# Performance work log

Hardware: AMD Instinct MI355X
Metric: run time of the kernel (lower is better)

Reference implementation:

```python
import jax, jax.numpy as jnp
import numpy as np

N_NODES = 50000
N_EDGES = 800000
NODE_DIM = 128
EDGE_LBL_DIM = 64
EDGE_FT_OUT_DIM = 128


def setup_inputs() -> dict:
    key = jax.random.key(0)
    k1, k2, k3, k4, k5 = jax.random.split(key, 5)
    h = jax.random.normal(k1, (N_NODES, NODE_DIM), dtype=jnp.float32)
    edge_labels = jax.random.normal(k2, (N_EDGES, EDGE_LBL_DIM), dtype=jnp.float32)
    src = jax.random.randint(k3, (N_EDGES,), 0, N_NODES)
    # learned params: fc (no bias) and e_attn_fc (no bias)
    W_fc = jax.random.normal(k4, (EDGE_LBL_DIM, EDGE_FT_OUT_DIM), dtype=jnp.float32) * 0.05
    W_attn = jax.random.normal(k5, (NODE_DIM + EDGE_FT_OUT_DIM, 1), dtype=jnp.float32) * 0.05
    return {"h": h, "edge_labels": edge_labels, "W_fc": W_fc, "W_attn": W_attn, "src": src}


def reference(h, edge_labels, W_fc, W_attn, src):
    """Edge weighting with segmented softmax grouped by src node.

    e_weighted = fc(edge_labels)                       # [E, F]
    a = e_attn_fc(concat([e_weighted, h[src]]))        # [E, 1]
    e = leaky_relu(a)
    gamma = softmax(e) segmented over edges sharing the same src
    out = gamma * e_weighted                           # [E, F]
    """
    n_nodes = h.shape[0]
    e_w = edge_labels @ W_fc                      # [E, F]
    src_ft = h[src]                               # [E, D] gather
    z2 = jnp.concatenate([e_w, src_ft], axis=-1)  # [E, D+F]
    a = z2 @ W_attn                               # [E, 1]
    e = jax.nn.leaky_relu(a, negative_slope=0.01)
    # segmented (per-src-group) numerically-stable softmax
    m = jax.ops.segment_max(e, src, num_segments=n_nodes)   # [N, 1]
    ex = jnp.exp(e - m[src])
    den = jax.ops.segment_sum(ex, src, num_segments=n_nodes)  # [N, 1]
    gamma = ex / den[src]
    return gamma * e_w
```

## Files before the change

### kernel.cpp

```cpp
#include <hip/hip_runtime.h>

#define N_DIM 128
#define L_DIM 64
#define F_DIM 128

__device__ __forceinline__ float rlane(float x, int l) {
    return __int_as_float(__builtin_amdgcn_readlane(__float_as_int(x), l));
}

__global__ void k_prep(const float* __restrict__ Wfc,
                       const float* __restrict__ Wattn,
                       float* __restrict__ v) {
    int k = threadIdx.x;
    float acc = 0.f;
#pragma unroll 8
    for (int f = 0; f < F_DIM; ++f) acc += Wfc[k * F_DIM + f] * Wattn[f];
    v[k] = acc;
}

__global__ void k_u(const float* __restrict__ h,
                    const float* __restrict__ Wattn,
                    float* __restrict__ u, int N) {
    int lane = threadIdx.x & 63;
    int wid = (int)((blockIdx.x * (unsigned)blockDim.x + threadIdx.x) >> 6);
    int nw  = (int)((gridDim.x * (unsigned)blockDim.x) >> 6);
    float2 wa = *(const float2*)(Wattn + F_DIM + 2 * lane);
    for (int n = wid; n < N; n += nw) {
        float2 hv = *(const float2*)(h + (long)n * N_DIM + 2 * lane);
        float p = hv.x * wa.x + hv.y * wa.y;
#pragma unroll
        for (int off = 32; off > 0; off >>= 1) p += __shfl_xor(p, off, 64);
        if (lane == 0) u[n] = p;
    }
}

__global__ void __launch_bounds__(256) k_se(const float* __restrict__ el,
                                            const float* __restrict__ v,
                                            const float* __restrict__ u,
                                            const int* __restrict__ src,
                                            float* __restrict__ ex_out,
                                            float* __restrict__ den,
                                            int E) {
    const int lane = threadIdx.x & 63;
    const int j16  = lane & 15;
    const int grp  = lane >> 4;
    int wid = (int)((blockIdx.x * (unsigned)blockDim.x + threadIdx.x) >> 6);
    int nw  = (int)((gridDim.x * (unsigned)blockDim.x) >> 6);

    float4 v4 = *(const float4*)(v + 4 * j16);
    const int C = (E + 63) >> 6;

    for (int c = wid; c < C; c += nw) {
        const long e0 = (long)c * 64;
        const int my_e = (int)e0 + 4 * j16 + grp;
        const bool full = (e0 + 64 <= E);

        if (full) {
            int   sv = src[my_e];
            float uu = u[sv];
            float kept = 0.f;
            const float4* elv = (const float4*)(el + e0 * L_DIM);
#pragma unroll
            for (int j = 0; j < 16; ++j) {
                float4 q = elv[j * 64 + lane];
                float p = q.x * v4.x + q.y * v4.y + q.z * v4.z + q.w * v4.w;
                p += __shfl_xor(p, 1, 64);
                p += __shfl_xor(p, 2, 64);
                p += __shfl_xor(p, 4, 64);
                p += __shfl_xor(p, 8, 64);
                float ue = __shfl(uu, (grp << 4) | j, 64);
                float s  = p + ue;
                float ev = fmaxf(s, 0.01f * s);
                float exv = __expf(ev);
                kept = (j16 == j) ? exv : kept;
            }
            ex_out[my_e] = kept;
            atomicAdd(den + sv, kept);
        } else {
            for (int j = 0; j < 16; ++j) {
                long e = e0 + 4 * j + grp;
                if (e >= E) continue;
                const float4* row = (const float4*)(el + e * L_DIM);
                float4 q = row[j16];
                float p = q.x * v4.x + q.y * v4.y + q.z * v4.z + q.w * v4.w;
                p += __shfl_xor(p, 1, 64);
                p += __shfl_xor(p, 2, 64);
                p += __shfl_xor(p, 4, 64);
                p += __shfl_xor(p, 8, 64);
                if (j16 == 0) {
                    int sv2 = src[e];
                    float s = p + u[sv2];
                    float ev = fmaxf(s, 0.01f * s);
                    float exv = __expf(ev);
                    ex_out[e] = exv;
                    atomicAdd(den + sv2, exv);
                }
            }
        }
    }
}

__global__ void __launch_bounds__(256, 1) k_out(const float* __restrict__ el,
                                                const float* __restrict__ Wfc,
                                                const int* __restrict__ src,
                                                const float* __restrict__ ex,
                                                const float* __restrict__ den,
                                                float* __restrict__ out,
                                                int E) {
    const int lane = threadIdx.x & 63;
    const int gw = (int)(blockIdx.x * 4u + (threadIdx.x >> 6));
    const int nw = (int)(gridDim.x * 4u);
    const int G = E >> 2;

    float w0[L_DIM], w1[L_DIM];
#pragma unroll
    for (int k = 0; k < L_DIM; ++k) {
        float2 wv = *(const float2*)(Wfc + k * F_DIM + 2 * lane);
        w0[k] = wv.x;
        w1[k] = wv.y;
    }

    int g = gw;
    if (g >= G) return;

    int gu = __builtin_amdgcn_readfirstlane(g);
    float4 q  = *(const float4*)(el + (long)gu * (4 * L_DIM) + lane * 4);
    float4 x4 = *(const float4*)(ex + 4 * (long)gu);
    int4   s4 = *(const int4*)(src + 4 * (long)gu);

    while (true) {
        const int gn = g + nw;
        const bool more = gn < G;
        float4 qn, x4n; int4 s4n;
        if (more) {
            int gun = __builtin_amdgcn_readfirstlane(gn);
            qn  = *(const float4*)(el + (long)gun * (4 * L_DIM) + lane * 4);
            x4n = *(const float4*)(ex + 4 * (long)gun);
            s4n = *(const int4*)(src + 4 * (long)gun);
        }
        float d0 = den[s4.x], d1 = den[s4.y], d2 = den[s4.z], d3 = den[s4.w];

        float a00 = 0.f, a01 = 0.f, a10 = 0.f, a11 = 0.f;
        float a20 = 0.f, a21 = 0.f, a30 = 0.f, a31 = 0.f;
        const float qa[4] = {q.x, q.y, q.z, q.w};
#pragma unroll
        for (int k = 0; k < L_DIM; ++k) {
            const int ln = k >> 2;
            const float c = qa[k & 3];
            float b0 = rlane(c, ln);
            float b1 = rlane(c, 16 + ln);
            float b2 = rlane(c, 32 + ln);
            float b3 = rlane(c, 48 + ln);
            a00 += b0 * w0[k]; a01 += b0 * w1[k];
            a10 += b1 * w0[k]; a11 += b1 * w1[k];
            a20 += b2 * w0[k]; a21 += b2 * w1[k];
            a30 += b3 * w0[k]; a31 += b3 * w1[k];
        }

        const float g0 = x4.x / d0, g1 = x4.y / d1;
        const float g2 = x4.z / d2, g3 = x4.w / d3;
        const long eb = (long)g * 4;
        *(float2*)(out + (eb + 0) * F_DIM + 2 * lane) = make_float2(g0 * a00, g0 * a01);
        *(float2*)(out + (eb + 1) * F_DIM + 2 * lane) = make_float2(g1 * a10, g1 * a11);
        *(float2*)(out + (eb + 2) * F_DIM + 2 * lane) = make_float2(g2 * a20, g2 * a21);
        *(float2*)(out + (eb + 3) * F_DIM + 2 * lane) = make_float2(g3 * a30, g3 * a31);

        if (!more) break;
        g = gn; q = qn; x4 = x4n; s4 = s4n;
    }
}

extern "C" void kernel_launch(void* const* d_in, const int* in_sizes, int n_in,
                              void* d_out, int out_size, void* d_ws, size_t ws_size,
                              hipStream_t stream) {
    const float* h     = (const float*)d_in[0];
    const float* el    = (const float*)d_in[1];
    const float* Wfc   = (const float*)d_in[2];
    const float* Wattn = (const float*)d_in[3];
    const int*   src   = (const int*)d_in[4];
    float* out = (float*)d_out;

    int N = in_sizes[0] / N_DIM;
    int E = in_sizes[4];

    float* v_ws = (float*)d_ws;
    float* u_ws = (float*)d_ws + 64;
    float* den  = (float*)d_ws + 64 + N;
    float* exb  = (float*)d_ws + 64 + 2 * (size_t)N;

    hipMemsetAsync(den, 0, (size_t)N * sizeof(float), stream);

    k_prep<<<1, 64, 0, stream>>>(Wfc, Wattn, v_ws);
    k_u<<<1024, 256, 0, stream>>>(h, Wattn, u_ws, N);
    k_se<<<1024, 256, 0, stream>>>(el, v_ws, u_ws, src, exb, den, E);
    k_out<<<2048, 256, 0, stream>>>(el, Wfc, src, exb, den, out, E);
}
```

Measured before the change: 744.3 us.

## Replicate softmax denominators per XCC and stage edge rows through LDS

Softmax denominator accumulation now goes to one replica per XCC, using workgroup-scope relaxed atomics, and a new merge kernel sums the replicas. This is meant to cut cross-die atomic contention. The output GEMV now broadcasts edge-label rows through double-buffered LDS instead of 256 readlane operations per group, and the launch-bounds occupancy hint is dropped. The weight-vector precompute is folded into the u kernel, which removes a launch. The risks are the extra merge pass and larger memset, and the assumption that workgroup-scope atomics stay coherent within an XCC.

Measured after the change: 917.6 us. 23.3% more time.

```diff
diff --git a/kernel.cpp b/kernel.cpp
--- a/kernel.cpp
+++ b/kernel.cpp
@@ -3,24 +3,26 @@
 #define N_DIM 128
 #define L_DIM 64
 #define F_DIM 128
-
-__device__ __forceinline__ float rlane(float x, int l) {
-    return __int_as_float(__builtin_amdgcn_readlane(__float_as_int(x), l));
-}
-
-__global__ void k_prep(const float* __restrict__ Wfc,
-                       const float* __restrict__ Wattn,
-                       float* __restrict__ v) {
-    int k = threadIdx.x;
-    float acc = 0.f;
+#define NREP 8
+
+__device__ __forceinline__ int xcc_id() {
+    int x;
+    asm volatile("s_getreg_b32 %0, hwreg(HW_REG_XCC_ID)" : "=s"(x));
+    return x & (NREP - 1);
+}
+
+__global__ void k_u(const float* __restrict__ h,
+                    const float* __restrict__ Wfc,
+                    const float* __restrict__ Wattn,
+                    float* __restrict__ u,
+                    float* __restrict__ v, int N) {
+    if (blockIdx.x == 0 && threadIdx.x < 64) {
+        int k = threadIdx.x;
+        float acc = 0.f;
 #pragma unroll 8
-    for (int f = 0; f < F_DIM; ++f) acc += Wfc[k * F_DIM + f] * Wattn[f];
-    v[k] = acc;
-}
-
-__global__ void k_u(const float* __restrict__ h,
-                    const float* __restrict__ Wattn,
-                    float* __restrict__ u, int N) {
+        for (int f = 0; f < F_DIM; ++f) acc += Wfc[k * F_DIM + f] * Wattn[f];
+        v[k] = acc;
+    }
     int lane = threadIdx.x & 63;
     int wid = (int)((blockIdx.x * (unsigned)blockDim.x + threadIdx.x) >> 6);
     int nw  = (int)((gridDim.x * (unsigned)blockDim.x) >> 6);
@@ -39,13 +41,15 @@
                                             const float* __restrict__ u,
                                             const int* __restrict__ src,
                                             float* __restrict__ ex_out,
-                                            float* __restrict__ den,
-                                            int E) {
+                                            float* __restrict__ den_rep,
+                                            int E, int N) {
     const int lane = threadIdx.x & 63;
     const int j16  = lane & 15;
     const int grp  = lane >> 4;
     int wid = (int)((blockIdx.x * (unsigned)blockDim.x + threadIdx.x) >> 6);
     int nw  = (int)((gridDim.x * (unsigned)blockDim.x) >> 6);
+
+    float* myrep = den_rep + (size_t)xcc_id() * N;
 
     float4 v4 = *(const float4*)(v + 4 * j16);
     const int C = (E + 63) >> 6;
@@ -75,7 +79,8 @@
                 kept = (j16 == j) ? exv : kept;
             }
             ex_out[my_e] = kept;
-            atomicAdd(den + sv, kept);
+            __hip_atomic_fetch_add(myrep + sv, kept, __ATOMIC_RELAXED,
+                                   __HIP_MEMORY_SCOPE_WORKGROUP);
         } else {
             for (int j = 0; j < 16; ++j) {
                 long e = e0 + 4 * j + grp;
@@ -93,22 +98,35 @@
                     float ev = fmaxf(s, 0.01f * s);
                     float exv = __expf(ev);
                     ex_out[e] = exv;
-                    atomicAdd(den + sv2, exv);
+                    __hip_atomic_fetch_add(myrep + sv2, exv, __ATOMIC_RELAXED,
+                                           __HIP_MEMORY_SCOPE_WORKGROUP);
                 }
             }
         }
     }
 }
 
-__global__ void __launch_bounds__(256, 1) k_out(const float* __restrict__ el,
-                                                const float* __restrict__ Wfc,
-                                                const int* __restrict__ src,
-                                                const float* __restrict__ ex,
-                                                const float* __restrict__ den,
-                                                float* __restrict__ out,
-                                                int E) {
+__global__ void k_merge(const float* __restrict__ rep,
+                        float* __restrict__ den, int N) {
+    int i = (int)(blockIdx.x * (unsigned)blockDim.x + threadIdx.x);
+    if (i >= N) return;
+    float s = 0.f;
+#pragma unroll
+    for (int r = 0; r < NREP; ++r) s += rep[(size_t)r * N + i];
+    den[i] = s;
+}
+
+__global__ void __launch_bounds__(256) k_out(const float* __restrict__ el,
+                                             const float* __restrict__ Wfc,
+                                             const int* __restrict__ src,
+                                             const float* __restrict__ ex,
+                                             const float* __restrict__ den,
+                                             float* __restrict__ out,
+                                             int E) {
+    __shared__ float4 sle[2][4][4][16];
     const int lane = threadIdx.x & 63;
-    const int gw = (int)(blockIdx.x * 4u + (threadIdx.x >> 6));
+    const int w    = threadIdx.x >> 6;
+    const int gw = (int)(blockIdx.x * 4u + w);
     const int nw = (int)(gridDim.x * 4u);
     const int G = E >> 2;
 
@@ -123,40 +141,42 @@
     int g = gw;
     if (g >= G) return;
 
-    int gu = __builtin_amdgcn_readfirstlane(g);
-    float4 q  = *(const float4*)(el + (long)gu * (4 * L_DIM) + lane * 4);
-    float4 x4 = *(const float4*)(ex + 4 * (long)gu);
-    int4   s4 = *(const int4*)(src + 4 * (long)gu);
+    float4 q = *(const float4*)(el + (long)g * (4 * L_DIM) + lane * 4);
+    int buf = 0;
+    sle[buf][w][lane >> 4][lane & 15] = q;
 
     while (true) {
         const int gn = g + nw;
         const bool more = gn < G;
-        float4 qn, x4n; int4 s4n;
+        float4 qn;
         if (more) {
-            int gun = __builtin_amdgcn_readfirstlane(gn);
-            qn  = *(const float4*)(el + (long)gun * (4 * L_DIM) + lane * 4);
-            x4n = *(const float4*)(ex + 4 * (long)gun);
-            s4n = *(const int4*)(src + 4 * (long)gun);
+            qn = *(const float4*)(el + (long)gn * (4 * L_DIM) + lane * 4);
         }
-        float d0 = den[s4.x], d1 = den[s4.y], d2 = den[s4.z], d3 = den[s4.w];
+        float4 x4 = *(const float4*)(ex + 4 * (long)g);
+        int4   s4 = *(const int4*)(src + 4 * (long)g);
 
         float a00 = 0.f, a01 = 0.f, a10 = 0.f, a11 = 0.f;
         float a20 = 0.f, a21 = 0.f, a30 = 0.f, a31 = 0.f;
-        const float qa[4] = {q.x, q.y, q.z, q.w};
-#pragma unroll
-        for (int k = 0; k < L_DIM; ++k) {
-            const int ln = k >> 2;
-            const float c = qa[k & 3];
-            float b0 = rlane(c, ln);
-            float b1 = rlane(c, 16 + ln);
-            float b2 = rlane(c, 32 + ln);
-            float b3 = rlane(c, 48 + ln);
-            a00 += b0 * w0[k]; a01 += b0 * w1[k];
-            a10 += b1 * w0[k]; a11 += b1 * w1[k];
-            a20 += b2 * w0[k]; a21 += b2 * w1[k];
-            a30 += b3 * w0[k]; a31 += b3 * w1[k];
+#pragma unroll
+        for (int k4 = 0; k4 < 16; ++k4) {
+            float4 b0 = sle[buf][w][0][k4];
+            float4 b1 = sle[buf][w][1][k4];
+            float4 b2 = sle[buf][w][2][k4];
+            float4 b3 = sle[buf][w][3][k4];
+            const int k = 4 * k4;
+            a00 += b0.x * w0[k] + b0.y * w0[k+1] + b0.z * w0[k+2] + b0.w * w0[k+3];
+            a01 += b0.x * w1[k] + b0.y * w1[k+1] + b0.z * w1[k+2] + b0.w * w1[k+3];
+            a10 += b1.x * w0[k] + b1.y * w0[k+1] + b1.z * w0[k+2] + b1.w * w0[k+3];
+            a11 += b1.x * w1[k] + b1.y * w1[k+1] + b1.z * w1[k+2] + b1.w * w1[k+3];
+            a20 += b2.x * w0[k] + b2.y * w0[k+1] + b2.z * w0[k+2] + b2.w * w0[k+3];
+            a21 += b2.x * w1[k] + b2.y * w1[k+1] + b2.z * w1[k+2] + b2.w * w1[k+3];
+            a30 += b3.x * w0[k] + b3.y * w0[k+1] + b3.z * w0[k+2] + b3.w * w0[k+3];
+            a31 += b3.x * w1[k] + b3.y * w1[k+1] + b3.z * w1[k+2] + b3.w * w1[k+3];
         }
 
+        if (more) sle[buf ^ 1][w][lane >> 4][lane & 15] = qn;
+
+        float d0 = den[s4.x], d1 = den[s4.y], d2 = den[s4.z], d3 = den[s4.w];
         const float g0 = x4.x / d0, g1 = x4.y / d1;
         const float g2 = x4.z / d2, g3 = x4.w / d3;
         const long eb = (long)g * 4;
@@ -166,7 +186,8 @@
         *(float2*)(out + (eb + 3) * F_DIM + 2 * lane) = make_float2(g3 * a30, g3 * a31);
 
         if (!more) break;
-        g = gn; q = qn; x4 = x4n; s4 = s4n;
+        g = gn;
+        buf ^= 1;
     }
 }
 
@@ -187,11 +208,12 @@
     float* u_ws = (float*)d_ws + 64;
     float* den  = (float*)d_ws + 64 + N;
     float* exb  = (float*)d_ws + 64 + 2 * (size_t)N;
-
-    hipMemsetAsync(den, 0, (size_t)N * sizeof(float), stream);
-
-    k_prep<<<1, 64, 0, stream>>>(Wfc, Wattn, v_ws);
-    k_u<<<1024, 256, 0, stream>>>(h, Wattn, u_ws, N);
-    k_se<<<1024, 256, 0, stream>>>(el, v_ws, u_ws, src, exb, den, E);
+    float* drep = (float*)d_ws + 64 + 2 * (size_t)N + E;
+
+    hipMemsetAsync(drep, 0, (size_t)NREP * N * sizeof(float), stream);
+
+    k_u<<<1024, 256, 0, stream>>>(h, Wfc, Wattn, u_ws, v_ws, N);
+    k_se<<<1024, 256, 0, stream>>>(el, v_ws, u_ws, src, exb, drep, E, N);
+    k_merge<<<(N + 255) / 256, 256, 0, stream>>>(drep, den, N);
     k_out<<<2048, 256, 0, stream>>>(el, Wfc, src, exb, den, out, E);
 }
```
